# Optimization experiments

Hardware: AMD Instinct MI355X
Metric: run time of the kernel (lower is better)

The kernel has to match this reference:

```python
import jax, jax.numpy as jnp
import numpy as np

NUM_HEADS = 12
HEAD_SIZE = 64
N_EMBED = 768
SEQ_LEN = 2048
BATCH = 4


def setup_inputs() -> dict:
    key = jax.random.key(0)
    ks = jax.random.split(key, 7)
    s = 0.02
    x = jax.random.normal(ks[0], (BATCH, SEQ_LEN, N_EMBED), dtype=jnp.float32)
    # per-head bias-free q/k/v projections: [H, E, D]
    Wq = jax.random.normal(ks[1], (NUM_HEADS, N_EMBED, HEAD_SIZE), dtype=jnp.float32) * s
    Wk = jax.random.normal(ks[2], (NUM_HEADS, N_EMBED, HEAD_SIZE), dtype=jnp.float32) * s
    Wv = jax.random.normal(ks[3], (NUM_HEADS, N_EMBED, HEAD_SIZE), dtype=jnp.float32) * s
    # output projection: Linear(num_heads*head_size, n_embed)
    Wp = jax.random.normal(ks[4], (NUM_HEADS * HEAD_SIZE, N_EMBED), dtype=jnp.float32) * s
    bp = jax.random.normal(ks[5], (N_EMBED,), dtype=jnp.float32) * s
    return {"x": x, "Wq": Wq, "Wk": Wk, "Wv": Wv, "Wp": Wp, "bp": bp}


def reference(x, Wq, Wk, Wv, Wp, bp):
    B, S, E = x.shape
    scale = HEAD_SIZE ** -0.5
    # project all heads at once: [B,H,S,D]
    q = jnp.einsum("bse,hed->bhsd", x, Wq)
    k = jnp.einsum("bse,hed->bhsd", x, Wk)
    v = jnp.einsum("bse,hed->bhsd", x, Wv)
    # scaled dot-product scores [B,H,S,S] with causal mask
    scores = jnp.einsum("bhsd,bhtd->bhst", q, k) * scale
    causal = jnp.tril(jnp.ones((S, S), dtype=bool))
    scores = jnp.where(causal[None, None, :, :], scores, jnp.finfo(scores.dtype).min)
    attn = jax.nn.softmax(scores, axis=-1)
    out = jnp.einsum("bhst,bhtd->bhsd", attn, v)
    # concat heads along feature dim: [B,S,H*D]
    out = out.transpose(0, 2, 1, 3).reshape(B, S, NUM_HEADS * HEAD_SIZE)
    # final projection (dropout rate = 0.0)
    return out @ Wp + bp
```

## Files before the change

kernel.cpp:

```cpp
#include <hip/hip_runtime.h>
#include <hip/hip_bf16.h>


typedef __attribute__((ext_vector_type(8))) short bf16x8;
typedef __attribute__((ext_vector_type(4))) float f32x4;
typedef __attribute__((ext_vector_type(16))) float f32x16;
typedef __attribute__((ext_vector_type(4))) uint u32x4;

#define OFF_XB   0
#define OFF_WT   6291456
#define OFF_WPT  8060928
#define OFF_QKV  8650752
#define OFF_AO   27525120

#define SCALE_LOG2E 0.1803368801111204f

__device__ inline ushort f2bf(float f) {
  __hip_bfloat16 h = __float2bfloat16(f);
  return *reinterpret_cast<ushort*>(&h);
}
__device__ inline uint cvt_pk(float lo, float hi) {
  uint r;
  asm("v_cvt_pk_bf16_f32 %0, %1, %2" : "=v"(r) : "v"(lo), "v"(hi));
  return r;
}
#define GLOAD16(g, l)                                                              \
  __builtin_amdgcn_global_load_lds(                                                \
      (const __attribute__((address_space(1))) uint*)(g),                          \
      (__attribute__((address_space(3))) uint*)(l), 16, 0, 0)

__global__ __launch_bounds__(256) void cvt_bf16(const float* __restrict__ src,
                                                ushort* __restrict__ dst, int n8) {
  int i = blockIdx.x * 256 + threadIdx.x;
  if (i >= n8) return;
  float4 a = *(const float4*)&src[(size_t)i * 8];
  float4 b = *(const float4*)&src[(size_t)i * 8 + 4];
  u32x4 pk = {cvt_pk(a.x, a.y), cvt_pk(a.z, a.w), cvt_pk(b.x, b.y), cvt_pk(b.z, b.w)};
  *(bf16x8*)&dst[(size_t)i * 8] = __builtin_bit_cast(bf16x8, pk);
}

__global__ __launch_bounds__(256) void transpose_w(const float* __restrict__ src,
                                                   ushort* __restrict__ dst,
                                                   int Edim, int Ddim) {
  __shared__ ushort tile[64][130];
  int mat = blockIdx.y;
  int ntd = Ddim >> 6;
  int te = blockIdx.x / ntd, td = blockIdx.x % ntd;
  size_t base = (size_t)mat * Edim * Ddim;
  int t = threadIdx.x;
#pragma unroll
  for (int i = 0; i < 16; i++) {
    int idx = i * 256 + t;
    int r = idx >> 6, c = idx & 63;
    tile[r][c] = f2bf(src[base + (size_t)(te * 64 + r) * Ddim + td * 64 + c]);
  }
  __syncthreads();
#pragma unroll
  for (int i = 0; i < 16; i++) {
    int idx = i * 256 + t;
    int c = idx >> 6, r = idx & 63;
    dst[base + (size_t)(td * 64 + c) * Edim + te * 64 + r] = tile[r][c];
  }
}

__device__ inline uint swz(uint row) { return (row + (row >> 2)) & 3; }

__global__ __launch_bounds__(256) void gemm_qkv(const ushort* __restrict__ X,
                                                const ushort* __restrict__ Wt,
                                                ushort* __restrict__ qkv,
                                                uint* __restrict__ vtg) {
  __shared__ ushort Ash[128 * 32];
  __shared__ ushort Bsh[128 * 32];
  int mb = blockIdx.x, nb = blockIdx.y;
  int t = threadIdx.x, w = t >> 6, lane = t & 63, lo = lane & 15, g = lane >> 4;
  int wr = w >> 1, wc = w & 1;
  const ushort* Ab = X + (size_t)mb * 128 * 768;
  const ushort* Bb = Wt + (size_t)nb * 128 * 768;
  f32x4 acc[4][4];
#pragma unroll
  for (int fi = 0; fi < 4; fi++)
#pragma unroll
    for (int fj = 0; fj < 4; fj++) acc[fi][fj] = (f32x4){0.f, 0.f, 0.f, 0.f};
  uint rsw = swz(lo) << 4;
  for (int e0 = 0; e0 < 768; e0 += 32) {
#pragma unroll
    for (int j = 0; j < 2; j++) {
      uint ci = w * 128 + j * 64 + lane;
      uint row = ci >> 2, c = ci & 3;
      uint sc = (c ^ swz(row)) << 4;
      GLOAD16((const char*)(Ab + (size_t)row * 768 + e0) + sc, Ash + (w * 128 + j * 64) * 8);
      GLOAD16((const char*)(Bb + (size_t)row * 768 + e0) + sc, Bsh + (w * 128 + j * 64) * 8);
    }
    __syncthreads();
    bf16x8 af[4], bf[4];
#pragma unroll
    for (int fi = 0; fi < 4; fi++) {
      int arow = wr * 64 + fi * 16 + lo;
      af[fi] = *(const bf16x8*)((const char*)Ash + arow * 64 + (((g << 4) ^ rsw)));
      int brow = wc * 64 + fi * 16 + lo;
      bf[fi] = *(const bf16x8*)((const char*)Bsh + brow * 64 + (((g << 4) ^ rsw)));
    }
#pragma unroll
    for (int fi = 0; fi < 4; fi++)
#pragma unroll
      for (int fj = 0; fj < 4; fj++)
        acc[fi][fj] = __builtin_amdgcn_mfma_f32_16x16x32_bf16(af[fi], bf[fj], acc[fi][fj], 0, 0, 0);
    __syncthreads();
  }
  int mat = nb * 2 + wc;
  int ty = mat / 12, h = mat % 12;
  if (ty < 2) {
#pragma unroll
    for (int fi = 0; fi < 4; fi++)
#pragma unroll
      for (int fj = 0; fj < 4; fj++) {
        int d = fj * 16 + lo;
#pragma unroll
        for (int rr = 0; rr < 4; rr++) {
          int m = mb * 128 + wr * 64 + fi * 16 + g * 4 + rr;
          int b = m >> 11, s = m & 2047;
          qkv[(size_t)ty * 6291456 + (size_t)(b * 12 + h) * 131072 + (size_t)s * 64 + d] =
              f2bf(acc[fi][fj][rr]);
        }
      }
  } else {
#pragma unroll
    for (int fi = 0; fi < 4; fi++)
#pragma unroll
      for (int fj = 0; fj < 4; fj++) {
        int d = fj * 16 + lo;
#pragma unroll
        for (int rr = 0; rr < 4; rr += 2) {
          int m = mb * 128 + wr * 64 + fi * 16 + g * 4 + rr;
          int b = m >> 11, s = m & 2047;
          uint pk = cvt_pk(acc[fi][fj][rr], acc[fi][fj][rr + 1]);
          vtg[(size_t)(b * 12 + h) * 65536 + (s >> 6) * 2048 + d * 32 + ((s & 63) >> 1)] = pk;
        }
      }
  }
}

__global__ __launch_bounds__(256, 3) void attn_fwd(const ushort* __restrict__ Qg,
                                                   const ushort* __restrict__ Kg,
                                                   const uint* __restrict__ Vtg,
                                                   ushort* __restrict__ ao) {
  __shared__ ushort Ksh[2][64 * 72];
  __shared__ uint Vsh[2][64 * 36];
  int x = blockIdx.x;
  int head = x % 48;
  int qb = 15 - x / 48;
  int T = 2 * qb + 2;
  int t = threadIdx.x, w = t >> 6, q31 = t & 31, hi = (t & 63) >> 5;
  const ushort* Q = Qg + (size_t)head * 131072;
  const ushort* K = Kg + (size_t)head * 131072;
  const uint* V = Vtg + (size_t)head * 65536;
  int qstart = qb * 128 + 32 * w;
  int qg = qstart + q31;
  bf16x8 qf[4];
#pragma unroll
  for (int s = 0; s < 4; s++)
    qf[s] = *(const bf16x8*)&Q[(size_t)qg * 64 + s * 16 + hi * 8];
  bf16x8 ones;
#pragma unroll
  for (int i = 0; i < 8; i++) ones[i] = (short)0x3F80;
  f32x16 oacc[2], lacc;
#pragma unroll
  for (int r = 0; r < 16; r++) { oacc[0][r] = 0.f; oacc[1][r] = 0.f; lacc[r] = 0.f; }
  int sr = t >> 3, sc = t & 7;
  bf16x8 kreg[2];
  u32x4 vreg[2];
#pragma unroll
  for (int i = 0; i < 2; i++) {
    kreg[i] = *(const bf16x8*)&K[(size_t)(i * 32 + sr) * 64 + sc * 8];
    vreg[i] = *(const u32x4*)&V[(i * 32 + sr) * 32 + sc * 4];
  }
#pragma unroll
  for (int i = 0; i < 2; i++) {
    *(bf16x8*)&Ksh[0][(i * 32 + sr) * 72 + sc * 8] = kreg[i];
    *(u32x4*)&Vsh[0][(i * 32 + sr) * 36 + sc * 4] = vreg[i];
  }
  for (int kb = 0; kb < T; kb++) {
    __syncthreads();
    if (kb + 1 < T) {
      int t1 = (kb + 1) * 64;
#pragma unroll
      for (int i = 0; i < 2; i++) {
        kreg[i] = *(const bf16x8*)&K[(size_t)(t1 + i * 32 + sr) * 64 + sc * 8];
        vreg[i] = *(const u32x4*)&V[(kb + 1) * 2048 + (i * 32 + sr) * 32 + sc * 4];
      }
    }
    int t0 = kb * 64;
    if (t0 <= qstart + 31) {
      const ushort* Kb = Ksh[kb & 1];
      const uint* Vb = Vsh[kb & 1];
      bool act1 = (t0 + 32 <= qstart + 31);
      f32x16 st0, st1;
#pragma unroll
      for (int r = 0; r < 16; r++) { st0[r] = 0.f; st1[r] = 0.f; }
#pragma unroll
      for (int s = 0; s < 4; s++) {
        bf16x8 kf = *(const bf16x8*)&Kb[q31 * 72 + s * 16 + hi * 8];
        st0 = __builtin_amdgcn_mfma_f32_32x32x16_bf16(kf, qf[s], st0, 0, 0, 0);
      }
      if (act1) {
#pragma unroll
        for (int s = 0; s < 4; s++) {
          bf16x8 kf = *(const bf16x8*)&Kb[(32 + q31) * 72 + s * 16 + hi * 8];
          st1 = __builtin_amdgcn_mfma_f32_32x32x16_bf16(kf, qf[s], st1, 0, 0, 0);
        }
      }
      if (t0 + 31 > qstart) {
        int base = t0 - qstart;
#pragma unroll
        for (int r = 0; r < 16; r++) {
          int crow = (r & 3) + 8 * (r >> 2) + 4 * hi;
          if (base + crow > q31) st0[r] = -3e38f;
        }
      }
      if (act1 && (t0 + 63 > qstart)) {
        int base = t0 + 32 - qstart;
#pragma unroll
        for (int r = 0; r < 16; r++) {
          int crow = (r & 3) + 8 * (r >> 2) + 4 * hi;
          if (base + crow > q31) st1[r] = -3e38f;
        }
      }
#pragma unroll
      for (int r = 0; r < 16; r++)
        st0[r] = __builtin_amdgcn_exp2f(st0[r] * SCALE_LOG2E);
      if (act1) {
#pragma unroll
        for (int r = 0; r < 16; r++)
          st1[r] = __builtin_amdgcn_exp2f(st1[r] * SCALE_LOG2E);
      }
      int ns = act1 ? 4 : 2;
      bf16x8 paf[4];
#pragma unroll
      for (int s = 0; s < 4; s++) {
        if (s < ns) {
          const f32x16& sv = (s < 2) ? st0 : st1;
          int rb = (s & 1) * 8;
          uint a = cvt_pk(sv[rb + 0], sv[rb + 1]);
          uint b2 = cvt_pk(sv[rb + 2], sv[rb + 3]);
          uint c = cvt_pk(sv[rb + 4], sv[rb + 5]);
          uint d = cvt_pk(sv[rb + 6], sv[rb + 7]);
          asm volatile("v_permlane32_swap_b32 %0, %1" : "+v"(a), "+v"(c));
          asm volatile("v_permlane32_swap_b32 %0, %1" : "+v"(b2), "+v"(d));
          u32x4 u4 = {a, b2, c, d};
          paf[s] = __builtin_bit_cast(bf16x8, u4);
        }
      }
#pragma unroll
      for (int s = 0; s < 4; s++) {
        if (s < ns) {
          lacc = __builtin_amdgcn_mfma_f32_32x32x16_bf16(paf[s], ones, lacc, 0, 0, 0);
#pragma unroll
          for (int dt = 0; dt < 2; dt++) {
            bf16x8 vf = *(const bf16x8*)&Vb[(dt * 32 + q31) * 36 + s * 8 + hi * 4];
            oacc[dt] = __builtin_amdgcn_mfma_f32_32x32x16_bf16(paf[s], vf, oacc[dt], 0, 0, 0);
          }
        }
      }
    }
    if (kb + 1 < T) {
      int b2 = (kb + 1) & 1;
#pragma unroll
      for (int i = 0; i < 2; i++) {
        *(bf16x8*)&Ksh[b2][(i * 32 + sr) * 72 + sc * 8] = kreg[i];
        *(u32x4*)&Vsh[b2][(i * 32 + sr) * 36 + sc * 4] = vreg[i];
      }
    }
  }
  int hh = head % 12, bb = head / 12;
#pragma unroll
  for (int dt = 0; dt < 2; dt++)
#pragma unroll
    for (int r = 0; r < 16; r++) {
      int qr = qstart + (r & 3) + 8 * (r >> 2) + 4 * hi;
      ao[(size_t)(bb * 2048 + qr) * 768 + hh * 64 + dt * 32 + q31] =
          f2bf(oacc[dt][r] / lacc[r]);
    }
}

__global__ __launch_bounds__(128) void gemm_out(const ushort* __restrict__ A,
                                                const ushort* __restrict__ Bt,
                                                const float* __restrict__ bias,
                                                float* __restrict__ out) {
  __shared__ ushort Ash[128 * 32];
  __shared__ ushort Bsh[64 * 32];
  int mb = blockIdx.x, nb = blockIdx.y;
  int t = threadIdx.x, w = t >> 6, lane = t & 63, lo = lane & 15, g = lane >> 4;
  const ushort* Ab = A + (size_t)mb * 128 * 768;
  const ushort* Bb = Bt + (size_t)nb * 64 * 768;
  f32x4 acc[4][4];
#pragma unroll
  for (int fi = 0; fi < 4; fi++)
#pragma unroll
    for (int fj = 0; fj < 4; fj++) acc[fi][fj] = (f32x4){0.f, 0.f, 0.f, 0.f};
  uint rsw = swz(lo) << 4;
  for (int e0 = 0; e0 < 768; e0 += 32) {
#pragma unroll
    for (int j = 0; j < 4; j++) {
      uint ci = w * 256 + j * 64 + lane;
      uint row = ci >> 2, c = ci & 3;
      uint sc = (c ^ swz(row)) << 4;
      GLOAD16((const char*)(Ab + (size_t)row * 768 + e0) + sc, Ash + (w * 256 + j * 64) * 8);
    }
#pragma unroll
    for (int j = 0; j < 2; j++) {
      uint ci = w * 128 + j * 64 + lane;
      uint row = ci >> 2, c = ci & 3;
      uint sc = (c ^ swz(row)) << 4;
      GLOAD16((const char*)(Bb + (size_t)row * 768 + e0) + sc, Bsh + (w * 128 + j * 64) * 8);
    }
    __syncthreads();
    bf16x8 af[4], bf[4];
#pragma unroll
    for (int fi = 0; fi < 4; fi++) {
      int arow = w * 64 + fi * 16 + lo;
      af[fi] = *(const bf16x8*)((const char*)Ash + arow * 64 + ((g << 4) ^ rsw));
      int brow = fi * 16 + lo;
      bf[fi] = *(const bf16x8*)((const char*)Bsh + brow * 64 + ((g << 4) ^ rsw));
    }
#pragma unroll
    for (int fi = 0; fi < 4; fi++)
#pragma unroll
      for (int fj = 0; fj < 4; fj++)
        acc[fi][fj] = __builtin_amdgcn_mfma_f32_16x16x32_bf16(af[fi], bf[fj], acc[fi][fj], 0, 0, 0);
    __syncthreads();
  }
#pragma unroll
  for (int fj = 0; fj < 4; fj++) {
    int col = nb * 64 + fj * 16 + lo;
    float bv = bias[col];
#pragma unroll
    for (int fi = 0; fi < 4; fi++)
#pragma unroll
      for (int rr = 0; rr < 4; rr++) {
        int m = mb * 128 + w * 64 + fi * 16 + g * 4 + rr;
        out[(size_t)m * 768 + col] = acc[fi][fj][rr] + bv;
      }
  }
}

extern "C" void kernel_launch(void* const* d_in, const int* in_sizes, int n_in,
                              void* d_out, int out_size, void* d_ws, size_t ws_size,
                              hipStream_t stream) {
  const float* x  = (const float*)d_in[0];
  const float* Wq = (const float*)d_in[1];
  const float* Wk = (const float*)d_in[2];
  const float* Wv = (const float*)d_in[3];
  const float* Wp = (const float*)d_in[4];
  const float* bp = (const float*)d_in[5];
  float* out = (float*)d_out;
  ushort* ws = (ushort*)d_ws;

  ushort* xb  = ws + OFF_XB;
  ushort* wt  = ws + OFF_WT;
  ushort* wpt = ws + OFF_WPT;
  ushort* qkv = ws + OFF_QKV;
  uint*   vt  = (uint*)(ws + OFF_QKV + 2 * 6291456);
  ushort* ao  = ws + OFF_AO;

  cvt_bf16<<<dim3(3072), 256, 0, stream>>>(x, xb, 786432);
  transpose_w<<<dim3(12, 12), 256, 0, stream>>>(Wq, wt + 0 * 589824, 768, 64);
  transpose_w<<<dim3(12, 12), 256, 0, stream>>>(Wk, wt + 1 * 589824, 768, 64);
  transpose_w<<<dim3(12, 12), 256, 0, stream>>>(Wv, wt + 2 * 589824, 768, 64);
  transpose_w<<<dim3(144, 1), 256, 0, stream>>>(Wp, wpt, 768, 768);

  gemm_qkv<<<dim3(64, 18), 256, 0, stream>>>(xb, wt, qkv, vt);
  attn_fwd<<<dim3(768), 256, 0, stream>>>(qkv, qkv + 6291456, vt, ao);
  gemm_out<<<dim3(64, 12), 128, 0, stream>>>(ao, wpt, bp, out);
}
```

Measured before the change: 144.4 us.

## Double-buffer LDS tiles in QKV and output GEMMs with async prefetch

Both projection GEMMs now keep two shared-memory tile buffers and issue the global-to-LDS loads for tile it+2 while computing on tile it. Each iteration waits only for the older tile's loads using vmcnt-based waits and raw barriers. This targets the load latency previously exposed by the load-sync-compute-sync loop. The cost is double the LDS footprint, which may lower occupancy, plus reliance on hand-written waitcnt accounting for correctness.

Result: faster. 133.7 us (-7.4%).

```diff
diff --git a/kernel.cpp b/kernel.cpp
--- a/kernel.cpp
+++ b/kernel.cpp
@@ -28,6 +28,9 @@
   __builtin_amdgcn_global_load_lds(                                                \
       (const __attribute__((address_space(1))) uint*)(g),                          \
       (__attribute__((address_space(3))) uint*)(l), 16, 0, 0)
+
+#define WAITBAR(n) asm volatile("s_waitcnt vmcnt(" #n ")\ns_barrier" ::: "memory")
+#define ENDBAR()   asm volatile("s_waitcnt lgkmcnt(0)\ns_barrier" ::: "memory")
 
 __global__ __launch_bounds__(256) void cvt_bf16(const float* __restrict__ src,
                                                 ushort* __restrict__ dst, int n8) {
@@ -69,8 +72,8 @@
                                                 const ushort* __restrict__ Wt,
                                                 ushort* __restrict__ qkv,
                                                 uint* __restrict__ vtg) {
-  __shared__ ushort Ash[128 * 32];
-  __shared__ ushort Bsh[128 * 32];
+  __shared__ ushort Ash[2][128 * 32];
+  __shared__ ushort Bsh[2][128 * 32];
   int mb = blockIdx.x, nb = blockIdx.y;
   int t = threadIdx.x, w = t >> 6, lane = t & 63, lo = lane & 15, g = lane >> 4;
   int wr = w >> 1, wc = w & 1;
@@ -81,32 +84,45 @@
   for (int fi = 0; fi < 4; fi++)
 #pragma unroll
     for (int fj = 0; fj < 4; fj++) acc[fi][fj] = (f32x4){0.f, 0.f, 0.f, 0.f};
+  uint ci0 = w * 128 + lane, ci1 = w * 128 + 64 + lane;
+  uint row0 = ci0 >> 2, sc0 = ((ci0 & 3) ^ swz(ci0 >> 2)) << 4;
+  uint row1 = ci1 >> 2, sc1 = ((ci1 & 3) ^ swz(ci1 >> 2)) << 4;
+
+#define QKV_STAGE(tile, bsel)                                                        \
+  {                                                                                  \
+    int e0 = (tile) * 32;                                                            \
+    GLOAD16((const char*)(Ab + (size_t)row0 * 768 + e0) + sc0, &Ash[bsel][(w * 128) * 8]);      \
+    GLOAD16((const char*)(Bb + (size_t)row0 * 768 + e0) + sc0, &Bsh[bsel][(w * 128) * 8]);      \
+    GLOAD16((const char*)(Ab + (size_t)row1 * 768 + e0) + sc1, &Ash[bsel][(w * 128 + 64) * 8]); \
+    GLOAD16((const char*)(Bb + (size_t)row1 * 768 + e0) + sc1, &Bsh[bsel][(w * 128 + 64) * 8]); \
+  }
+
+  QKV_STAGE(0, 0);
+  QKV_STAGE(1, 1);
   uint rsw = swz(lo) << 4;
-  for (int e0 = 0; e0 < 768; e0 += 32) {
-#pragma unroll
-    for (int j = 0; j < 2; j++) {
-      uint ci = w * 128 + j * 64 + lane;
-      uint row = ci >> 2, c = ci & 3;
-      uint sc = (c ^ swz(row)) << 4;
-      GLOAD16((const char*)(Ab + (size_t)row * 768 + e0) + sc, Ash + (w * 128 + j * 64) * 8);
-      GLOAD16((const char*)(Bb + (size_t)row * 768 + e0) + sc, Bsh + (w * 128 + j * 64) * 8);
-    }
-    __syncthreads();
+  for (int it = 0; it < 24; ++it) {
+    if (it < 23) { WAITBAR(4); } else { WAITBAR(0); }
+    const ushort* Acur = Ash[it & 1];
+    const ushort* Bcur = Bsh[it & 1];
     bf16x8 af[4], bf[4];
 #pragma unroll
     for (int fi = 0; fi < 4; fi++) {
       int arow = wr * 64 + fi * 16 + lo;
-      af[fi] = *(const bf16x8*)((const char*)Ash + arow * 64 + (((g << 4) ^ rsw)));
+      af[fi] = *(const bf16x8*)((const char*)Acur + arow * 64 + ((g << 4) ^ rsw));
       int brow = wc * 64 + fi * 16 + lo;
-      bf[fi] = *(const bf16x8*)((const char*)Bsh + brow * 64 + (((g << 4) ^ rsw)));
+      bf[fi] = *(const bf16x8*)((const char*)Bcur + brow * 64 + ((g << 4) ^ rsw));
     }
 #pragma unroll
     for (int fi = 0; fi < 4; fi++)
 #pragma unroll
       for (int fj = 0; fj < 4; fj++)
         acc[fi][fj] = __builtin_amdgcn_mfma_f32_16x16x32_bf16(af[fi], bf[fj], acc[fi][fj], 0, 0, 0);
-    __syncthreads();
-  }
+    if (it < 22) {
+      ENDBAR();
+      QKV_STAGE(it + 2, it & 1);
+    }
+  }
+#undef QKV_STAGE
   int mat = nb * 2 + wc;
   int ty = mat / 12, h = mat % 12;
   if (ty < 2) {
@@ -286,8 +302,8 @@
                                                 const ushort* __restrict__ Bt,
                                                 const float* __restrict__ bias,
                                                 float* __restrict__ out) {
-  __shared__ ushort Ash[128 * 32];
-  __shared__ ushort Bsh[64 * 32];
+  __shared__ ushort Ash[2][128 * 32];
+  __shared__ ushort Bsh[2][64 * 32];
   int mb = blockIdx.x, nb = blockIdx.y;
   int t = threadIdx.x, w = t >> 6, lane = t & 63, lo = lane & 15, g = lane >> 4;
   const ushort* Ab = A + (size_t)mb * 128 * 768;
@@ -297,38 +313,59 @@
   for (int fi = 0; fi < 4; fi++)
 #pragma unroll
     for (int fj = 0; fj < 4; fj++) acc[fi][fj] = (f32x4){0.f, 0.f, 0.f, 0.f};
+  uint aci[4], asc[4], bci[2], bsc[2];
+#pragma unroll
+  for (int j = 0; j < 4; j++) {
+    uint ci = w * 256 + j * 64 + lane;
+    aci[j] = ci;
+    asc[j] = ((ci & 3) ^ swz(ci >> 2)) << 4;
+  }
+#pragma unroll
+  for (int j = 0; j < 2; j++) {
+    uint ci = w * 128 + j * 64 + lane;
+    bci[j] = ci;
+    bsc[j] = ((ci & 3) ^ swz(ci >> 2)) << 4;
+  }
+
+#define OUT_STAGE(tile, bsel)                                                          \
+  {                                                                                    \
+    int e0 = (tile) * 32;                                                              \
+    _Pragma("unroll")                                                                  \
+    for (int j = 0; j < 4; j++)                                                        \
+      GLOAD16((const char*)(Ab + (size_t)(aci[j] >> 2) * 768 + e0) + asc[j],           \
+              &Ash[bsel][(w * 256 + j * 64) * 8]);                                     \
+    _Pragma("unroll")                                                                  \
+    for (int j = 0; j < 2; j++)                                                        \
+      GLOAD16((const char*)(Bb + (size_t)(bci[j] >> 2) * 768 + e0) + bsc[j],           \
+              &Bsh[bsel][(w * 128 + j * 64) * 8]);                                     \
+  }
+
+  OUT_STAGE(0, 0);
+  OUT_STAGE(1, 1);
   uint rsw = swz(lo) << 4;
-  for (int e0 = 0; e0 < 768; e0 += 32) {
-#pragma unroll
-    for (int j = 0; j < 4; j++) {
-      uint ci = w * 256 + j * 64 + lane;
-      uint row = ci >> 2, c = ci & 3;
-      uint sc = (c ^ swz(row)) << 4;
-      GLOAD16((const char*)(Ab + (size_t)row * 768 + e0) + sc, Ash + (w * 256 + j * 64) * 8);
-    }
-#pragma unroll
-    for (int j = 0; j < 2; j++) {
-      uint ci = w * 128 + j * 64 + lane;
-      uint row = ci >> 2, c = ci & 3;
-      uint sc = (c ^ swz(row)) << 4;
-      GLOAD16((const char*)(Bb + (size_t)row * 768 + e0) + sc, Bsh + (w * 128 + j * 64) * 8);
-    }
-    __syncthreads();
+  for (int it = 0; it < 24; ++it) {
+    if (it < 23) { WAITBAR(6); } else { WAITBAR(0); }
+    const ushort* Acur = Ash[it & 1];
+    const ushort* Bcur = Bsh[it & 1];
     bf16x8 af[4], bf[4];
 #pragma unroll
     for (int fi = 0; fi < 4; fi++) {
       int arow = w * 64 + fi * 16 + lo;
-      af[fi] = *(const bf16x8*)((const char*)Ash + arow * 64 + ((g << 4) ^ rsw));
+      af[fi] = *(const bf16x8*)((const char*)Acur + arow * 64 + ((g << 4) ^ rsw));
       int brow = fi * 16 + lo;
-      bf[fi] = *(const bf16x8*)((const char*)Bsh + brow * 64 + ((g << 4) ^ rsw));
+      bf[fi] = *(const bf16x8*)((const char*)Bcur + brow * 64 + ((g << 4) ^ rsw));
     }
 #pragma unroll
     for (int fi = 0; fi < 4; fi++)
 #pragma unroll
       for (int fj = 0; fj < 4; fj++)
         acc[fi][fj] = __builtin_amdgcn_mfma_f32_16x16x32_bf16(af[fi], bf[fj], acc[fi][fj], 0, 0, 0);
-    __syncthreads();
-  }
+    if (it < 22) {
+      ENDBAR();
+      OUT_STAGE(it + 2, it & 1);
+    }
+  }
+#undef OUT_STAGE
 #pragma unroll
   for (int fj = 0; fj < 4; fj++) {
     int col = nb * 64 + fj * 16 + lo;
```
